# Performance work log

Measured on AMD Instinct MI355X. Metric: run time of the kernel, lower is better.

Reference implementation:

```python
import jax, jax.numpy as jnp
import numpy as np

B, S, D = 4, 8192, 1024   # batch, seq_len, d_model
DG = 256                  # genre embedding dim
E, K = 64, 2              # n_experts, top_k


def setup_inputs() -> dict:
    key = jax.random.key(0)
    k1, k2, k3, k4 = jax.random.split(key, 4)
    x = jax.random.normal(k1, (B, S, D), dtype=jnp.float32)
    genre_emb = jax.random.normal(k2, (B, DG), dtype=jnp.float32)
    # router parameters (kaiming-ish scale)
    Wx = jax.random.normal(k3, (D, E), dtype=jnp.float32) / np.sqrt(D)
    Wg = jax.random.normal(k4, (DG, E), dtype=jnp.float32) / np.sqrt(DG)
    b = jnp.zeros((E,), dtype=jnp.float32)
    return {"x": x, "genre_emb": genre_emb, "Wx": Wx, "Wg": Wg, "b": b}


def reference(x, genre_emb, Wx, Wg, b):
    # Router logits conditioned on token state and broadcast genre embedding.
    # x: [B,S,D], genre_emb: [B,DG] -> logits [B,S,E]
    logits = jnp.einsum("bsd,de->bse", x, Wx) + (genre_emb @ Wg)[:, None, :] + b
    probs = jax.nn.softmax(logits, axis=-1)          # [B,S,E]
    topk_vals, topk_idx = jax.lax.top_k(probs, K)    # [B,S,K]
    # renormalize selected expert weights to sum to 1
    topk_vals = topk_vals / topk_vals.sum(axis=-1, keepdims=True)
    # scatter back to sparse dense gate tensor [B,S,E]
    onehot = jax.nn.one_hot(topk_idx, E, dtype=topk_vals.dtype)  # [B,S,K,E]
    gates = jnp.einsum("bsk,bske->bse", topk_vals, onehot)
    return gates, topk_idx
```

## Files before the change

### kernel.cpp

```cpp
#include <hip/hip_runtime.h>
#include <math.h>

#define NTOK   32768
#define DMODEL 1024
#define NEXP   64
#define DGENRE 256
#define BK     64
#define TT     64
#define XSTR   68

__global__ void genre_bias_k(const float* __restrict__ genre,
                             const float* __restrict__ Wg,
                             const float* __restrict__ bias,
                             float* __restrict__ c) {
  int tid = threadIdx.x;
  int b = tid >> 6, e = tid & 63;
  float acc = bias[e];
  const float* g = genre + b * DGENRE;
  for (int d = 0; d < DGENRE; ++d) acc = fmaf(g[d], Wg[d * NEXP + e], acc);
  c[b * NEXP + e] = acc;
}

__device__ __forceinline__ bool better(float va, int ia, float vb, int ib) {
  return (va > vb) || (va == vb && ia < ib);
}

__global__ __launch_bounds__(256, 2) void moe_gate_k(
    const float* __restrict__ x, const float* __restrict__ Wx,
    const float* __restrict__ c, float* __restrict__ out) {
  __shared__ float xs[BK][XSTR];
  __shared__ float wss[BK][NEXP];

  const int tid  = threadIdx.x;
  const int tok0 = blockIdx.x * TT;

  const int eg = tid & 15;
  const int tg = tid >> 4;
  const int e0 = eg * 4;
  const int t0 = tg * 4;

  const int lq = tid & 15;
  const int lr = tid >> 4;

  float acc[4][4] = {{0.f}};

  for (int d0 = 0; d0 < DMODEL; d0 += BK) {
    __syncthreads();
#pragma unroll
    for (int l = 0; l < 4; ++l) {
      int t = lr + l * 16;
      float4 v = *reinterpret_cast<const float4*>(
          &x[(size_t)(tok0 + t) * DMODEL + d0 + lq * 4]);
      xs[lq * 4 + 0][t] = v.x;
      xs[lq * 4 + 1][t] = v.y;
      xs[lq * 4 + 2][t] = v.z;
      xs[lq * 4 + 3][t] = v.w;
    }
#pragma unroll
    for (int l = 0; l < 4; ++l) {
      int r = lr + l * 16;
      *reinterpret_cast<float4*>(&wss[r][lq * 4]) =
          *reinterpret_cast<const float4*>(&Wx[(size_t)(d0 + r) * NEXP + lq * 4]);
    }
    __syncthreads();
#pragma unroll 8
    for (int d = 0; d < BK; ++d) {
      float4 xv = *reinterpret_cast<const float4*>(&xs[d][t0]);
      float4 wv = *reinterpret_cast<const float4*>(&wss[d][e0]);
      float xa[4] = {xv.x, xv.y, xv.z, xv.w};
      float wa[4] = {wv.x, wv.y, wv.z, wv.w};
#pragma unroll
      for (int i = 0; i < 4; ++i)
#pragma unroll
        for (int j = 0; j < 4; ++j)
          acc[i][j] = fmaf(xa[i], wa[j], acc[i][j]);
    }
  }

  const int b = tok0 >> 13;
#pragma unroll
  for (int j = 0; j < 4; ++j) {
    float cb = c[b * NEXP + e0 + j];
#pragma unroll
    for (int i = 0; i < 4; ++i) acc[i][j] += cb;
  }

  float* gates  = out;
  float* idxout = out + (size_t)NTOK * NEXP;

#pragma unroll
  for (int i = 0; i < 4; ++i) {
    float v1 = acc[i][0]; int i1 = e0;
    float v2 = -INFINITY; int i2 = NEXP;
#pragma unroll
    for (int j = 1; j < 4; ++j) {
      float a = acc[i][j]; int ei = e0 + j;
      if (better(a, ei, v1, i1)) { v2 = v1; i2 = i1; v1 = a; i1 = ei; }
      else if (better(a, ei, v2, i2)) { v2 = a; i2 = ei; }
    }
#pragma unroll
    for (int m = 1; m < 16; m <<= 1) {
      float ov1 = __shfl_xor(v1, m, 64); int oi1 = __shfl_xor(i1, m, 64);
      float ov2 = __shfl_xor(v2, m, 64); int oi2 = __shfl_xor(i2, m, 64);
      if (better(v1, i1, ov1, oi1)) {
        if (better(ov1, oi1, v2, i2)) { v2 = ov1; i2 = oi1; }
      } else {
        if (better(v1, i1, ov2, oi2)) { v2 = v1; i2 = i1; }
        else                          { v2 = ov2; i2 = oi2; }
        v1 = ov1; i1 = oi1;
      }
    }
    float ew  = expf(v2 - v1);
    float inv = 1.0f / (1.0f + ew);
    float w1 = inv, w2 = ew * inv;

    int tok = tok0 + t0 + i;
    float4 g;
    g.x = (e0 + 0 == i1) ? w1 : ((e0 + 0 == i2) ? w2 : 0.0f);
    g.y = (e0 + 1 == i1) ? w1 : ((e0 + 1 == i2) ? w2 : 0.0f);
    g.z = (e0 + 2 == i1) ? w1 : ((e0 + 2 == i2) ? w2 : 0.0f);
    g.w = (e0 + 3 == i1) ? w1 : ((e0 + 3 == i2) ? w2 : 0.0f);
    *reinterpret_cast<float4*>(&gates[(size_t)tok * NEXP + e0]) = g;

    if (eg == 0) {
      idxout[(size_t)tok * 2 + 0] = (float)i1;
      idxout[(size_t)tok * 2 + 1] = (float)i2;
    }
  }
}

extern "C" void kernel_launch(void* const* d_in, const int* in_sizes, int n_in,
                              void* d_out, int out_size, void* d_ws, size_t ws_size,
                              hipStream_t stream) {
  const float* x     = (const float*)d_in[0];
  const float* genre = (const float*)d_in[1];
  const float* Wx    = (const float*)d_in[2];
  const float* Wg    = (const float*)d_in[3];
  const float* bias  = (const float*)d_in[4];
  float* out = (float*)d_out;
  float* c   = (float*)d_ws;

  genre_bias_k<<<1, 256, 0, stream>>>(genre, Wg, bias, c);
  moe_gate_k<<<NTOK / TT, 256, 0, stream>>>(x, Wx, c, out);
}
```

Baseline: 242.9 us.

## Double-buffer tiles via direct global-to-LDS loads and fuse genre bias

Replaces the register-staged, transposed shared-memory fill with async global_load_lds copies into double-buffered LDS tiles. The x tile now keeps its row-major layout with an XOR swizzle to avoid bank conflicts, and the next tile is prefetched while the current one is computed. The separate genre-bias kernel is folded into the main kernel: each block recomputes the genre bias for its batch. This removes one launch and overlaps memory with compute, at the cost of redundant per-block bias work and more LDS per block.

```diff
diff --git a/kernel.cpp b/kernel.cpp
--- a/kernel.cpp
+++ b/kernel.cpp
@@ -7,19 +7,9 @@
 #define DGENRE 256
 #define BK     64
 #define TT     64
-#define XSTR   68
 
-__global__ void genre_bias_k(const float* __restrict__ genre,
-                             const float* __restrict__ Wg,
-                             const float* __restrict__ bias,
-                             float* __restrict__ c) {
-  int tid = threadIdx.x;
-  int b = tid >> 6, e = tid & 63;
-  float acc = bias[e];
-  const float* g = genre + b * DGENRE;
-  for (int d = 0; d < DGENRE; ++d) acc = fmaf(g[d], Wg[d * NEXP + e], acc);
-  c[b * NEXP + e] = acc;
-}
+typedef const __attribute__((address_space(1))) void ga_void;
+typedef __attribute__((address_space(3))) void lds_void;
 
 __device__ __forceinline__ bool better(float va, int ia, float vb, int ib) {
   return (va > vb) || (va == vb && ia < ib);
@@ -27,60 +17,97 @@
 
 __global__ __launch_bounds__(256, 2) void moe_gate_k(
     const float* __restrict__ x, const float* __restrict__ Wx,
-    const float* __restrict__ c, float* __restrict__ out) {
-  __shared__ float xs[BK][XSTR];
-  __shared__ float wss[BK][NEXP];
+    const float* __restrict__ genre, const float* __restrict__ Wg,
+    const float* __restrict__ bias, float* __restrict__ out) {
+  __shared__ __align__(16) float xs[2][TT * BK];
+  __shared__ __align__(16) float ws[2][BK * NEXP];
+  __shared__ float cpart[4][NEXP];
+  __shared__ float cbias[NEXP];
 
   const int tid  = threadIdx.x;
+  const int wv   = tid >> 6;
+  const int lane = tid & 63;
   const int tok0 = blockIdx.x * TT;
+  const int b    = tok0 >> 13;
+
+  {
+    const int e = tid & 63, dc = tid >> 6;
+    const float* g  = genre + b * DGENRE + dc * 64;
+    const float* wg = Wg + (size_t)(dc * 64) * NEXP + e;
+    float p = 0.f;
+#pragma unroll 8
+    for (int d = 0; d < 64; ++d) p = fmaf(g[d], wg[(size_t)d * NEXP], p);
+    cpart[dc][e] = p;
+  }
 
   const int eg = tid & 15;
   const int tg = tid >> 4;
   const int e0 = eg * 4;
   const int t0 = tg * 4;
-
-  const int lq = tid & 15;
-  const int lr = tid >> 4;
+  const int sw = tg & 3;
 
   float acc[4][4] = {{0.f}};
 
-  for (int d0 = 0; d0 < DMODEL; d0 += BK) {
-    __syncthreads();
-#pragma unroll
-    for (int l = 0; l < 4; ++l) {
-      int t = lr + l * 16;
-      float4 v = *reinterpret_cast<const float4*>(
-          &x[(size_t)(tok0 + t) * DMODEL + d0 + lq * 4]);
-      xs[lq * 4 + 0][t] = v.x;
-      xs[lq * 4 + 1][t] = v.y;
-      xs[lq * 4 + 2][t] = v.z;
-      xs[lq * 4 + 3][t] = v.w;
-    }
-#pragma unroll
-    for (int l = 0; l < 4; ++l) {
-      int r = lr + l * 16;
-      *reinterpret_cast<float4*>(&wss[r][lq * 4]) =
-          *reinterpret_cast<const float4*>(&Wx[(size_t)(d0 + r) * NEXP + lq * 4]);
-    }
-    __syncthreads();
-#pragma unroll 8
-    for (int d = 0; d < BK; ++d) {
-      float4 xv = *reinterpret_cast<const float4*>(&xs[d][t0]);
-      float4 wv = *reinterpret_cast<const float4*>(&wss[d][e0]);
-      float xa[4] = {xv.x, xv.y, xv.z, xv.w};
-      float wa[4] = {wv.x, wv.y, wv.z, wv.w};
-#pragma unroll
-      for (int i = 0; i < 4; ++i)
-#pragma unroll
-        for (int j = 0; j < 4; ++j)
-          acc[i][j] = fmaf(xa[i], wa[j], acc[i][j]);
-    }
+#define STAGE(bufidx, d0)                                                      \
+  {                                                                            \
+    _Pragma("unroll")                                                          \
+    for (int s = 0; s < 4; ++s) {                                              \
+      const int L = wv * 256 + s * 64 + lane;                                  \
+      const int t = L >> 4, pq = L & 15;                                       \
+      const int dq = pq ^ ((t >> 2) & 3);                                      \
+      const float* gsrc = x + (size_t)(tok0 + t) * DMODEL + (d0) + dq * 4;     \
+      __builtin_amdgcn_global_load_lds((ga_void*)gsrc,                         \
+          (lds_void*)&xs[bufidx][(wv * 256 + s * 64) * 4], 16, 0, 0);          \
+      const float* wsrc = Wx + (size_t)(d0) * NEXP + L * 4;                    \
+      __builtin_amdgcn_global_load_lds((ga_void*)wsrc,                         \
+          (lds_void*)&ws[bufidx][(wv * 256 + s * 64) * 4], 16, 0, 0);          \
+    }                                                                          \
   }
 
-  const int b = tok0 >> 13;
+#define COMPUTE(bufidx)                                                        \
+  {                                                                            \
+    const float* xb = &xs[bufidx][0];                                          \
+    const float* wb = &ws[bufidx][0];                                          \
+    _Pragma("unroll 4")                                                        \
+    for (int dq = 0; dq < 16; ++dq) {                                          \
+      float4 xv[4], wv4[4];                                                    \
+      _Pragma("unroll")                                                        \
+      for (int i = 0; i < 4; ++i)                                              \
+        xv[i] = *reinterpret_cast<const float4*>(                              \
+            &xb[(t0 + i) * BK + ((dq ^ sw) << 2)]);                            \
+      _Pragma("unroll")                                                        \
+      for (int dd = 0; dd < 4; ++dd)                                           \
+        wv4[dd] = *reinterpret_cast<const float4*>(                            \
+            &wb[(dq * 4 + dd) * NEXP + e0]);                                   \
+      _Pragma("unroll")                                                        \
+      for (int dd = 0; dd < 4; ++dd) {                                         \
+        _Pragma("unroll")                                                      \
+        for (int i = 0; i < 4; ++i) {                                          \
+          const float xvv = reinterpret_cast<const float*>(&xv[i])[dd];        \
+          _Pragma("unroll")                                                    \
+          for (int j = 0; j < 4; ++j)                                          \
+            acc[i][j] = fmaf(                                                  \
+                xvv, reinterpret_cast<const float*>(&wv4[dd])[j], acc[i][j]);  \
+        }                                                                      \
+      }                                                                        \
+    }                                                                          \
+  }
+
+  STAGE(0, 0);
+  __syncthreads();
+  if (tid < NEXP)
+    cbias[tid] = bias[tid] + cpart[0][tid] + cpart[1][tid] + cpart[2][tid] +
+                 cpart[3][tid];
+
+  for (int c = 0; c < DMODEL / BK; ++c) {
+    if (c < DMODEL / BK - 1) STAGE((c + 1) & 1, (c + 1) * BK);
+    COMPUTE(c & 1);
+    __syncthreads();
+  }
+
 #pragma unroll
   for (int j = 0; j < 4; ++j) {
-    float cb = c[b * NEXP + e0 + j];
+    const float cb = cbias[e0 + j];
 #pragma unroll
     for (int i = 0; i < 4; ++i) acc[i][j] += cb;
   }
@@ -94,14 +121,14 @@
     float v2 = -INFINITY; int i2 = NEXP;
 #pragma unroll
     for (int j = 1; j < 4; ++j) {
-      float a = acc[i][j]; int ei = e0 + j;
+      const float a = acc[i][j]; const int ei = e0 + j;
       if (better(a, ei, v1, i1)) { v2 = v1; i2 = i1; v1 = a; i1 = ei; }
       else if (better(a, ei, v2, i2)) { v2 = a; i2 = ei; }
     }
 #pragma unroll
     for (int m = 1; m < 16; m <<= 1) {
-      float ov1 = __shfl_xor(v1, m, 64); int oi1 = __shfl_xor(i1, m, 64);
-      float ov2 = __shfl_xor(v2, m, 64); int oi2 = __shfl_xor(i2, m, 64);
+      const float ov1 = __shfl_xor(v1, m, 64); const int oi1 = __shfl_xor(i1, m, 64);
+      const float ov2 = __shfl_xor(v2, m, 64); const int oi2 = __shfl_xor(i2, m, 64);
       if (better(v1, i1, ov1, oi1)) {
         if (better(ov1, oi1, v2, i2)) { v2 = ov1; i2 = oi1; }
       } else {
@@ -110,11 +137,11 @@
         v1 = ov1; i1 = oi1;
       }
     }
-    float ew  = expf(v2 - v1);
-    float inv = 1.0f / (1.0f + ew);
-    float w1 = inv, w2 = ew * inv;
+    const float ew  = expf(v2 - v1);
+    const float inv = 1.0f / (1.0f + ew);
+    const float w1 = inv, w2 = ew * inv;
 
-    int tok = tok0 + t0 + i;
+    const int tok = tok0 + t0 + i;
     float4 g;
     g.x = (e0 + 0 == i1) ? w1 : ((e0 + 0 == i2) ? w2 : 0.0f);
     g.y = (e0 + 1 == i1) ? w1 : ((e0 + 1 == i2) ? w2 : 0.0f);
@@ -138,8 +165,6 @@
   const float* Wg    = (const float*)d_in[3];
   const float* bias  = (const float*)d_in[4];
   float* out = (float*)d_out;
-  float* c   = (float*)d_ws;
 
-  genre_bias_k<<<1, 256, 0, stream>>>(genre, Wg, bias, c);
-  moe_gate_k<<<NTOK / TT, 256, 0, stream>>>(x, Wx, c, out);
+  moe_gate_k<<<NTOK / TT, 256, 0, stream>>>(x, Wx, genre, Wg, bias, out);
 }
```

Measured after the change: 222.6 us. 1.09x faster.
